# Performance work log

Hardware: AMD Instinct MI355X
Metric: run time of the kernel (lower is better)

Reference implementation:

```python
import jax, jax.numpy as jnp
import numpy as np

LOG2E = 1.4426950408889634  # 1/ln(2): convert natural-log gates to log2 space (kernel uses exp2)
BT = 64  # chunk size


def setup_inputs() -> dict:
    key = jax.random.key(0)
    ks = jax.random.split(key, 5)
    B, H, T, K, V = 4, 8, 4096, 128, 128
    return {
        "q": jax.random.normal(ks[0], (B, H, T, K), dtype=jnp.float32),
        "k": jax.random.normal(ks[1], (B, H, T, K), dtype=jnp.float32),
        "v": jax.random.normal(ks[2], (B, H, T, V), dtype=jnp.float32),
        "i_gate": jax.random.normal(ks[3], (B, H, T), dtype=jnp.float32),
        "f_gate": jax.random.normal(ks[4], (B, H, T), dtype=jnp.float32),
    }


def reference(q, k, v, i_gate, f_gate):
    B, H, T, K = q.shape
    V = v.shape[-1]
    NT = T // BT
    scale = K ** -0.5

    # gate preprocessing: log-sigmoid forget gate, both gates moved to log2 space
    vecF = jax.nn.log_sigmoid(f_gate) * LOG2E  # [B,H,T]
    vecI = i_gate * LOG2E                      # [B,H,T]

    f_c = vecF.reshape(B, H, NT, BT)
    i_c = vecI.reshape(B, H, NT, BT)
    qc = q.reshape(B, H, NT, BT, K)
    kc = k.reshape(B, H, NT, BT, K)
    vc = v.reshape(B, H, NT, BT, V)

    vecB = jnp.cumsum(f_c, axis=-1)            # inclusive cumsum of f within chunk [B,H,NT,BT]
    scaG = vecB[..., -1]                       # total decay per chunk [B,H,NT]
    vecA = i_c + (scaG[..., None] - vecB)      # i_j + sum of f after j within chunk

    # ---- inter-chunk recurrence over matrix state C, normalizer n, max m ----
    kx = jnp.moveaxis(kc, 2, 0)  # [NT,B,H,BT,K]
    vx = jnp.moveaxis(vc, 2, 0)
    ax = jnp.moveaxis(vecA, 2, 0)  # [NT,B,H,BT]
    gx = jnp.moveaxis(scaG, 2, 0)  # [NT,B,H]

    C0 = jnp.zeros((B, H, K, V), dtype=q.dtype)
    n0 = jnp.zeros((B, H, K), dtype=q.dtype)
    m0 = jnp.zeros((B, H), dtype=q.dtype)

    def step(carry, inp):
        C, n, m = carry
        kk, vv, a, g = inp
        m_next = jnp.maximum(g + m, jnp.max(a, axis=-1))      # running stabilizer max
        dec = jnp.exp2(g + m - m_next)                        # [B,H]
        kbar = kk * jnp.exp2(a - m_next[..., None])[..., None]
        C_next = C * dec[..., None, None] + jnp.einsum('bhtk,bhtv->bhkv', kbar, vv)
        n_next = n * dec[..., None] + kbar.sum(axis=-2)
        return (C_next, n_next, m_next), (C, n, m)

    _, (Cp, np_, mp) = jax.lax.scan(step, (C0, n0, m0), (kx, vx, ax, gx))
    Cp = jnp.moveaxis(Cp, 0, 2)   # state entering each chunk [B,H,NT,K,V]
    np_ = jnp.moveaxis(np_, 0, 2)  # [B,H,NT,K]
    mp = jnp.moveaxis(mp, 0, 2)   # [B,H,NT]

    # ---- intra-chunk parallel part ----
    idx = jnp.arange(BT)
    causal = idx[:, None] >= idx[None, :]  # query i attends key j<=i
    # logD[i,j] = B_i - B_j + I_j for j<=i
    logD = vecB[..., :, None] - vecB[..., None, :] + i_c[..., None, :]
    logD = jnp.where(causal, logD, -jnp.inf)
    m_intra = logD.max(axis=-1)                                   # [B,H,NT,BT]
    m_comb = jnp.maximum(mp[..., None] + vecB, m_intra)           # total stabilizer per row
    D = jnp.exp2(logD - m_comb[..., None])                        # masked entries -> 0

    S = jnp.einsum('bhcik,bhcjk->bhcij', qc, kc) * scale * D
    qbar = qc * (scale * jnp.exp2(vecB + mp[..., None] - m_comb))[..., None]

    Hnum = jnp.einsum('bhcik,bhckv->bhciv', qbar, Cp) + jnp.einsum('bhcij,bhcjv->bhciv', S, vc)
    den = jnp.einsum('bhcik,bhck->bhci', qbar, np_) + S.sum(axis=-1)
    norm = jnp.maximum(jnp.abs(den), jnp.exp2(-m_comb))
    h = Hnum / norm[..., None]
    return h.reshape(B, H, T, V)
```

## Files before the change

### kernel.cpp

```cpp
#include <hip/hip_runtime.h>
#include <hip/hip_bf16.h>
#include <math.h>


#define LOG2E 1.4426950408889634f
constexpr int Bsz = 4, Hsz = 8, Tsz = 4096, Ksz = 128, Vsz = 128;
constexpr int BT = 64, NT = 64, BH = Bsz * Hsz;
constexpr float SCALE = 0.08838834764831845f;
constexpr int CPB = 4;

typedef __attribute__((ext_vector_type(8))) short short8v;
typedef __attribute__((ext_vector_type(4))) float f32x4;
typedef __attribute__((ext_vector_type(4))) unsigned short u16x4;
typedef __attribute__((ext_vector_type(8))) unsigned short u16x8;

__device__ inline float bf2f(unsigned short u) {
    union { unsigned int i; float f; } c; c.i = ((unsigned int)u) << 16; return c.f;
}
__device__ inline unsigned short f2bf(float f) {
    __hip_bfloat16 h = __float2bfloat16(f);
    union { __hip_bfloat16 b; unsigned short u; } cv; cv.b = h; return cv.u;
}
__device__ inline float f4c(const float4& v, int y) {
    return y == 0 ? v.x : y == 1 ? v.y : y == 2 ? v.z : v.w;
}

__global__ __launch_bounds__(64) void k_gates(
    const float* __restrict__ ig, const float* __restrict__ fg,
    float* __restrict__ vecB, float* __restrict__ vecI, float* __restrict__ vecA,
    float* __restrict__ mintra, float* __restrict__ scaG, float* __restrict__ scaA)
{
    int c = blockIdx.x, bh = blockIdx.y, lane = threadIdx.x;
    int t = bh * Tsz + c * BT + lane;
    float f = fg[t];
    float ls = fminf(f, 0.f) - log1pf(expf(-fabsf(f)));
    float vF = ls * LOG2E;
    float vI = ig[t] * LOG2E;
    float b = vF;
    #pragma unroll
    for (int off = 1; off < 64; off <<= 1) {
        float o = __shfl_up(b, off, 64);
        if (lane >= off) b += o;
    }
    float g = __shfl(b, 63, 64);
    float mi = vI - b;
    #pragma unroll
    for (int off = 1; off < 64; off <<= 1) {
        float o = __shfl_up(mi, off, 64);
        if (lane >= off) mi = fmaxf(mi, o);
    }
    float a = vI + g - b;
    vecB[t] = b; vecI[t] = vI; vecA[t] = a; mintra[t] = b + mi;
    float am = a;
    #pragma unroll
    for (int off = 32; off; off >>= 1) am = fmaxf(am, __shfl_xor(am, off, 64));
    if (lane == 0) { scaG[bh * NT + c] = g; scaA[bh * NT + c] = am; }
}

__global__ __launch_bounds__(64) void k_mscan(
    const float* __restrict__ scaG, const float* __restrict__ scaA,
    float* __restrict__ mp, float* __restrict__ dec)
{
    int bh = blockIdx.x, lane = threadIdx.x;
    float g0 = scaG[bh * NT + lane];
    float a = g0, b = scaA[bh * NT + lane];
    #pragma unroll
    for (int off = 1; off < 64; off <<= 1) {
        float ap = __shfl_up(a, off, 64);
        float bp = __shfl_up(b, off, 64);
        if (lane >= off) { b = fmaxf(bp + a, b); a = ap + a; }
    }
    float m_incl = fmaxf(a, b);
    float m_prev = __shfl_up(m_incl, 1, 64);
    if (lane == 0) { m_prev = 0.f; mp[bh * (NT + 1)] = 0.f; }
    mp[bh * (NT + 1) + lane + 1] = m_incl;
    dec[bh * NT + lane] = exp2f(g0 + m_prev - m_incl);
}

__global__ __launch_bounds__(256, 2) void k_state(
    const float* __restrict__ kg, const float* __restrict__ vg,
    const float* __restrict__ vecA, const float* __restrict__ mp,
    unsigned short* __restrict__ UT, float* __restrict__ nU)
{
    int c0 = blockIdx.x * CPB, bh = blockIdx.y, tid = threadIdx.x;
    int lane = tid & 63, wid = tid >> 6;
    int lrow = lane & 15, kgrp = lane >> 4;

    __shared__ __align__(16) unsigned short kT[2][128][72];
    __shared__ __align__(16) unsigned short vT[2][128][72];
    __shared__ float nUp[2][128][5];

    int cb = tid & 15, jr = tid >> 4;
    int wboff = (((jr >> 1) ^ (cb & 7)) * 16) + (jr & 1) * 8;
    const float* mpb = mp + bh * (NT + 1);

    float4 kreg[4][2], vreg[4][2];

    auto issue_loads = [&](int cc) {
        size_t hbc = (size_t)bh * Tsz + (size_t)(c0 + cc) * BT;
        #pragma unroll
        for (int x = 0; x < 4; ++x)
            #pragma unroll
            for (int p = 0; p < 2; ++p) {
                kreg[x][p] = *(const float4*)(kg + (hbc + jr * 4 + x) * Ksz + p * 64 + cb * 4);
                vreg[x][p] = *(const float4*)(vg + (hbc + jr * 4 + x) * Vsz + p * 64 + cb * 4);
            }
    };
    auto cvt_store = [&](int cc, int b) {
        size_t hbc = (size_t)bh * Tsz + (size_t)(c0 + cc) * BT;
        float mpn = mpb[c0 + cc + 1];
        float s4[4];
        #pragma unroll
        for (int x = 0; x < 4; ++x) s4[x] = exp2f(vecA[hbc + jr * 4 + x] - mpn);
        #pragma unroll
        for (int p = 0; p < 2; ++p) {
            int cb0 = p * 64 + cb * 4;
            #pragma unroll
            for (int y = 0; y < 4; ++y) {
                u16x4 h, w;
                float psum = 0.f;
                #pragma unroll
                for (int x = 0; x < 4; ++x) {
                    float kf = f4c(kreg[x][p], y) * s4[x];
                    h[x] = f2bf(kf);
                    psum += kf;
                    w[x] = f2bf(f4c(vreg[x][p], y));
                }
                *(u16x4*)((char*)&kT[b][cb0 + y][0] + wboff) = h;
                *(u16x4*)((char*)&vT[b][cb0 + y][0] + wboff) = w;
                psum += __shfl_xor(psum, 16, 64);
                psum += __shfl_xor(psum, 32, 64);
                if (kgrp == 0) nUp[b][cb0 + y][wid] = psum;
            }
        }
    };

    issue_loads(0);
    cvt_store(0, 0);
    __syncthreads();

    int b = 0;
    for (int cc = 0; cc < CPB; ++cc) {
        if (cc + 1 < CPB) issue_loads(cc + 1);

        f32x4 acc[2][8];
        #pragma unroll
        for (int kt = 0; kt < 2; ++kt)
            #pragma unroll
            for (int vt = 0; vt < 8; ++vt) acc[kt][vt] = (f32x4){0.f, 0.f, 0.f, 0.f};
        #pragma unroll
        for (int ks = 0; ks < 2; ++ks) {
            int G = ks * 4 + kgrp;
            #pragma unroll
            for (int kt = 0; kt < 2; ++kt) {
                int arow = (wid * 2 + kt) * 16 + lrow;
                short8v af = *(const short8v*)((const char*)&kT[b][arow][0]
                                               + ((G ^ ((arow >> 2) & 7)) * 16));
                #pragma unroll
                for (int vt = 0; vt < 8; ++vt) {
                    int brow = vt * 16 + lrow;
                    short8v bv = *(const short8v*)((const char*)&vT[b][brow][0]
                                                   + ((G ^ ((brow >> 2) & 7)) * 16));
                    acc[kt][vt] = __builtin_amdgcn_mfma_f32_16x16x32_bf16(af, bv, acc[kt][vt], 0, 0, 0);
                }
            }
        }
        unsigned short* Ub = UT + (size_t)(bh * NT + c0 + cc) * (Ksz * Vsz);
        #pragma unroll
        for (int kt = 0; kt < 2; ++kt) {
            int ktile = wid * 2 + kt;
            #pragma unroll
            for (int vt = 0; vt < 8; ++vt) {
                u16x4 w;
                #pragma unroll
                for (int r = 0; r < 4; ++r) w[r] = f2bf(acc[kt][vt][r]);
                *(u16x4*)(Ub + ((size_t)(ktile * 8 + vt) * 64 + lane) * 4) = w;
            }
        }
        if (tid < Ksz) {
            float s = nUp[b][tid][0] + nUp[b][tid][1] + nUp[b][tid][2] + nUp[b][tid][3];
            nU[(size_t)(bh * NT + c0 + cc) * Ksz + tid] = s;
        }

        if (cc + 1 < CPB) {
            cvt_store(cc + 1, b ^ 1);
            __syncthreads();
            b ^= 1;
        }
    }
}

__global__ __launch_bounds__(128) void k_scan(
    unsigned short* __restrict__ UT, const float* __restrict__ dec,
    const float* __restrict__ nU, float* __restrict__ np)
{
    int s = blockIdx.x, bh = blockIdx.y, tid = threadIdx.x;
    __shared__ float decs[NT];
    if (tid < NT) decs[tid] = dec[bh * NT + tid];
    __syncthreads();
    if (s == 32) {
        float n = 0.f;
        size_t base = (size_t)bh * NT * Ksz + tid;
        #pragma unroll 4
        for (int c2 = 0; c2 < NT; ++c2) {
            float u = nU[base + (size_t)c2 * Ksz];
            np[base + (size_t)c2 * Ksz] = n;
            n = n * decs[c2] + u;
        }
        return;
    }
    size_t base = (size_t)bh * NT * (Ksz * Vsz) + s * 512 + tid * 4;
    float C0 = 0.f, C1 = 0.f, C2 = 0.f, C3 = 0.f;
    #pragma unroll 4
    for (int c2 = 0; c2 < NT; ++c2) {
        size_t idx = base + (size_t)c2 * (Ksz * Vsz);
        u16x4 u = *(const u16x4*)(UT + idx);
        u16x4 w;
        w.x = f2bf(C0); w.y = f2bf(C1); w.z = f2bf(C2); w.w = f2bf(C3);
        *(u16x4*)(UT + idx) = w;
        float d = decs[c2];
        C0 = C0 * d + bf2f(u.x); C1 = C1 * d + bf2f(u.y);
        C2 = C2 * d + bf2f(u.z); C3 = C3 * d + bf2f(u.w);
    }
}

__global__ __launch_bounds__(256, 4) void k_intra(
    const float* __restrict__ qg, const float* __restrict__ kgl, const float* __restrict__ vg,
    const float* __restrict__ vecB, const float* __restrict__ vecI,
    const float* __restrict__ mintra, const float* __restrict__ mp,
    const float* __restrict__ np, const unsigned short* __restrict__ CpT,
    float* __restrict__ out)
{
    int c = blockIdx.x, bh = blockIdx.y, tid = threadIdx.x;
    int lane = tid & 63, wid = tid >> 6;
    int lrow = lane & 15, kgrp = lane >> 4;

    __shared__ __align__(16) unsigned short R[17408];
    __shared__ float rowf[BT], colf[BT], sfqs[BT], emcs[BT], denb[BT], npv[Ksz];

    auto khi = (unsigned short(*)[136])R;
    auto klo = (unsigned short(*)[136])(R + 64 * 136);
    auto Sb  = (unsigned short(*)[72])R;
    unsigned short* vTf = R + 64 * 72;
    unsigned short* cpsF = R;

    size_t hb = (size_t)bh * Tsz + (size_t)c * BT;
    float mpc = mp[bh * (NT + 1) + c];
    if (tid < BT) {
        float b = vecB[hb + tid];
        float mc = fmaxf(mpc + b, mintra[hb + tid]);
        rowf[tid] = SCALE * exp2f(b - mc);
        colf[tid] = exp2f(vecI[hb + tid] - b);
        sfqs[tid] = SCALE * exp2f(b + mpc - mc);
        emcs[tid] = exp2f(-mc);
    }
    if (tid < Ksz) npv[tid] = np[((size_t)bh * NT + c) * Ksz + tid];

    const float4* k4 = (const float4*)(kgl + hb * Ksz);
    for (int e = tid; e < BT * Ksz / 4; e += 256) {
        int i = e >> 5, c4 = (e & 31) * 4;
        float4 kv = k4[e];
        u16x4 h, l;
        h.x = f2bf(kv.x); l.x = f2bf(kv.x - bf2f(h.x));
        h.y = f2bf(kv.y); l.y = f2bf(kv.y - bf2f(h.y));
        h.z = f2bf(kv.z); l.z = f2bf(kv.z - bf2f(h.z));
        h.w = f2bf(kv.w); l.w = f2bf(kv.w - bf2f(h.w));
        *(u16x4*)&khi[i][c4] = h; *(u16x4*)&klo[i][c4] = l;
    }
    const float* qrow = qg + (hb + wid * 16 + lrow) * Ksz;
    float qf[4][8];
    #pragma unroll
    for (int ks = 0; ks < 4; ++ks) {
        float4 a = *(const float4*)(qrow + ks * 32 + kgrp * 8);
        float4 b = *(const float4*)(qrow + ks * 32 + kgrp * 8 + 4);
        qf[ks][0] = a.x; qf[ks][1] = a.y; qf[ks][2] = a.z; qf[ks][3] = a.w;
        qf[ks][4] = b.x; qf[ks][5] = b.y; qf[ks][6] = b.z; qf[ks][7] = b.w;
    }
    int vcb = tid & 15, jb = tid >> 4;
    float vpre[2][4][4];
    #pragma unroll
    for (int p = 0; p < 2; ++p)
        #pragma unroll
        for (int x = 0; x < 4; ++x) {
            float4 r4 = *(const float4*)(vg + (hb + jb * 4 + x) * Vsz + p * 64 + vcb * 4);
            vpre[p][x][0] = r4.x; vpre[p][x][1] = r4.y; vpre[p][x][2] = r4.z; vpre[p][x][3] = r4.w;
        }
    __syncthreads();

    float dot = 0.f;
    #pragma unroll
    for (int ks = 0; ks < 4; ++ks)
        #pragma unroll
        for (int x = 0; x < 8; ++x) dot += qf[ks][x] * npv[ks * 32 + kgrp * 8 + x];
    dot += __shfl_xor(dot, 16, 64);
    dot += __shfl_xor(dot, 32, 64);
    float qdot = sfqs[wid * 16 + lrow] * dot;

    short8v qh[4], ql[4];
    #pragma unroll
    for (int ks = 0; ks < 4; ++ks)
        #pragma unroll
        for (int x = 0; x < 8; ++x) {
            float f = qf[ks][x];
            unsigned short hh = f2bf(f);
            qh[ks][x] = (short)hh;
            ql[ks][x] = (short)f2bf(f - bf2f(hh));
        }

    f32x4 accS[4];
    #pragma unroll
    for (int jt = 0; jt < 4; ++jt) accS[jt] = (f32x4){0.f, 0.f, 0.f, 0.f};
    #pragma unroll
    for (int ks = 0; ks < 4; ++ks) {
        #pragma unroll
        for (int jt = 0; jt < 4; ++jt) {
            if (jt <= wid) {
                short8v bh_ = *(const short8v*)&khi[jt * 16 + lrow][ks * 32 + kgrp * 8];
                short8v bl  = *(const short8v*)&klo[jt * 16 + lrow][ks * 32 + kgrp * 8];
                accS[jt] = __builtin_amdgcn_mfma_f32_16x16x32_bf16(qh[ks], bh_, accS[jt], 0, 0, 0);
                accS[jt] = __builtin_amdgcn_mfma_f32_16x16x32_bf16(ql[ks], bh_, accS[jt], 0, 0, 0);
                accS[jt] = __builtin_amdgcn_mfma_f32_16x16x32_bf16(qh[ks], bl,  accS[jt], 0, 0, 0);
            }
        }
    }

    float rsum[4] = {0.f, 0.f, 0.f, 0.f};
    unsigned short sreg[4][4];
    #pragma unroll
    for (int jt = 0; jt < 4; ++jt)
        #pragma unroll
        for (int r = 0; r < 4; ++r) {
            int i = wid * 16 + kgrp * 4 + r, j = jt * 16 + lrow;
            float val = (j <= i) ? accS[jt][r] * rowf[i] * colf[j] : 0.f;
            rsum[r] += val;
            sreg[jt][r] = f2bf(val);
        }
    #pragma unroll
    for (int r = 0; r < 4; ++r) {
        rsum[r] += __shfl_xor(rsum[r], 1, 64);
        rsum[r] += __shfl_xor(rsum[r], 2, 64);
        rsum[r] += __shfl_xor(rsum[r], 4, 64);
        rsum[r] += __shfl_xor(rsum[r], 8, 64);
    }
    float qd[4];
    #pragma unroll
    for (int r = 0; r < 4; ++r) qd[r] = __shfl(qdot, kgrp * 4 + r, 64);
    if (lrow == 0) {
        #pragma unroll
        for (int r = 0; r < 4; ++r) {
            int i = wid * 16 + kgrp * 4 + r;
            float den = qd[r] + rsum[r];
            denb[i] = 1.f / fmaxf(fabsf(den), emcs[i]);
        }
    }
    __syncthreads();

    const u16x8* Cg = (const u16x8*)(CpT + ((size_t)bh * NT + c) * (Ksz * Vsz));
    u16x8 cpre[8];
    #pragma unroll
    for (int p2 = 0; p2 < 8; ++p2) cpre[p2] = Cg[tid + p2 * 256];

    #pragma unroll
    for (int jt = 0; jt < 4; ++jt)
        #pragma unroll
        for (int r = 0; r < 4; ++r)
            Sb[wid * 16 + kgrp * 4 + r][jt * 16 + lrow] = sreg[jt][r];
    #pragma unroll
    for (int p = 0; p < 2; ++p)
        #pragma unroll
        for (int y = 0; y < 4; ++y) {
            int row = p * 64 + vcb * 4 + y;
            int swzb = (jb * 8) ^ ((row & 7) << 4);
            u16x4 w;
            #pragma unroll
            for (int x = 0; x < 4; ++x) w[x] = f2bf(vpre[p][x][y]);
            *(u16x4*)((char*)(vTf + row * 64) + swzb) = w;
        }
    __syncthreads();

    f32x4 accV[8];
    #pragma unroll
    for (int vt = 0; vt < 8; ++vt) accV[vt] = (f32x4){0.f, 0.f, 0.f, 0.f};
    #pragma unroll
    for (int ks = 0; ks < 2; ++ks) {
        short8v as_ = *(const short8v*)&Sb[wid * 16 + lrow][ks * 32 + kgrp * 8];
        #pragma unroll
        for (int vt = 0; vt < 8; ++vt) {
            int row = vt * 16 + lrow;
            int swzb = ((ks * 64 + kgrp * 16)) ^ ((row & 7) << 4);
            short8v bv = *(const short8v*)((const char*)(vTf + row * 64) + swzb);
            accV[vt] = __builtin_amdgcn_mfma_f32_16x16x32_bf16(as_, bv, accV[vt], 0, 0, 0);
        }
    }
    __syncthreads();

    #pragma unroll
    for (int p2 = 0; p2 < 8; ++p2) {
        int idx = tid + p2 * 256;
        *(u16x8*)&cpsF[idx * 8] = cpre[p2];
    }
    __syncthreads();

    f32x4 accC[8];
    #pragma unroll
    for (int vt = 0; vt < 8; ++vt) accC[vt] = (f32x4){0.f, 0.f, 0.f, 0.f};
    #pragma unroll
    for (int ks = 0; ks < 4; ++ks) {
        int ktile = ks * 2 + (kgrp >> 1);
        int lsrc = (kgrp & 1) * 32 + lrow;
        #pragma unroll
        for (int vt = 0; vt < 8; ++vt) {
            const unsigned short* pf = &cpsF[((ktile * 8 + vt) * 64 + lsrc) * 4];
            u16x4 lo4 = *(const u16x4*)pf;
            u16x4 hi4 = *(const u16x4*)(pf + 64);
            short8v bc;
            bc[0] = (short)lo4.x; bc[1] = (short)lo4.y; bc[2] = (short)lo4.z; bc[3] = (short)lo4.w;
            bc[4] = (short)hi4.x; bc[5] = (short)hi4.y; bc[6] = (short)hi4.z; bc[7] = (short)hi4.w;
            accC[vt] = __builtin_amdgcn_mfma_f32_16x16x32_bf16(qh[ks], bc, accC[vt], 0, 0, 0);
            accC[vt] = __builtin_amdgcn_mfma_f32_16x16x32_bf16(ql[ks], bc, accC[vt], 0, 0, 0);
        }
    }
    size_t gb = hb * Vsz;
    #pragma unroll
    for (int vt = 0; vt < 8; ++vt)
        #pragma unroll
        for (int r = 0; r < 4; ++r) {
            int i = wid * 16 + kgrp * 4 + r, vc = vt * 16 + lrow;
            out[gb + (size_t)i * Vsz + vc] = (sfqs[i] * accC[vt][r] + accV[vt][r]) * denb[i];
        }
}

extern "C" void kernel_launch(void* const* d_in, const int* in_sizes, int n_in,
                              void* d_out, int out_size, void* d_ws, size_t ws_size,
                              hipStream_t stream) {
    const float* q  = (const float*)d_in[0];
    const float* k  = (const float*)d_in[1];
    const float* v  = (const float*)d_in[2];
    const float* ig = (const float*)d_in[3];
    const float* fg = (const float*)d_in[4];
    float* out = (float*)d_out;

    float* ws = (float*)d_ws;
    float* vecB   = ws;
    float* vecI   = vecB + BH * Tsz;
    float* vecA   = vecI + BH * Tsz;
    float* mintra = vecA + BH * Tsz;
    float* scaG   = mintra + BH * Tsz;
    float* scaA   = scaG + BH * NT;
    float* dec    = scaA + BH * NT;
    float* mp     = dec + BH * NT;
    float* nU     = mp + BH * (NT + 1);
    float* np     = nU + BH * NT * Ksz;
    unsigned short* UT = (unsigned short*)(np + BH * NT * Ksz);

    k_gates<<<dim3(NT, BH), 64, 0, stream>>>(ig, fg, vecB, vecI, vecA, mintra, scaG, scaA);
    k_mscan<<<dim3(BH), 64, 0, stream>>>(scaG, scaA, mp, dec);
    k_state<<<dim3(NT / CPB, BH), 256, 0, stream>>>(k, v, vecA, mp, UT, nU);
    k_scan<<<dim3(33, BH), 128, 0, stream>>>(UT, dec, nU, np);
    k_intra<<<dim3(NT, BH), 256, 0, stream>>>(q, k, v, vecB, vecI, mintra, mp, np, UT, out);
}
```

Baseline: 124.9 us.

## Replace flat chunk-state scan with two-level grouped scan and in-block local recurrence

Each k_state block now runs the state recurrence across a group of 8 chunks in registers, emitting per-chunk local states and a group-total state. A short scan over 8 group states replaces the 64-step global scan, which removes the serial scan and its round-trip through the per-chunk update buffer. k_intra combines the local state with the decayed group prefix using precomputed decay factors. This costs a second state load and an extra 128x128 MFMA pass per chunk in k_intra, and k_state launches fewer blocks (8 per head instead of 16) with longer serial work, so there is less parallelism.

```diff
diff --git a/kernel.cpp b/kernel.cpp
--- a/kernel.cpp
+++ b/kernel.cpp
@@ -7,7 +7,7 @@
 constexpr int Bsz = 4, Hsz = 8, Tsz = 4096, Ksz = 128, Vsz = 128;
 constexpr int BT = 64, NT = 64, BH = Bsz * Hsz;
 constexpr float SCALE = 0.08838834764831845f;
-constexpr int CPB = 4;
+constexpr int GS = 8, NG = NT / GS;
 
 typedef __attribute__((ext_vector_type(8))) short short8v;
 typedef __attribute__((ext_vector_type(4))) float f32x4;
@@ -59,7 +59,8 @@
 
 __global__ __launch_bounds__(64) void k_mscan(
     const float* __restrict__ scaG, const float* __restrict__ scaA,
-    float* __restrict__ mp, float* __restrict__ dec)
+    float* __restrict__ mp, float* __restrict__ dec,
+    float* __restrict__ pdec, float* __restrict__ decG)
 {
     int bh = blockIdx.x, lane = threadIdx.x;
     float g0 = scaG[bh * NT + lane];
@@ -75,14 +76,28 @@
     if (lane == 0) { m_prev = 0.f; mp[bh * (NT + 1)] = 0.f; }
     mp[bh * (NT + 1) + lane + 1] = m_incl;
     dec[bh * NT + lane] = exp2f(g0 + m_prev - m_incl);
-}
-
-__global__ __launch_bounds__(256, 2) void k_state(
+    float cumE = a - g0;
+    int gs = lane & ~(GS - 1);
+    float cumE_gs = __shfl(cumE, gs, 64);
+    float mp_gs   = __shfl(m_prev, gs, 64);
+    pdec[bh * NT + lane] = exp2f(cumE - cumE_gs + mp_gs - m_prev);
+    int ge = (lane * GS) & 63, gl = (lane * GS + GS - 1) & 63;
+    float cumS = __shfl(cumE, ge, 64);
+    float mS   = __shfl(m_prev, ge, 64);
+    float cumL = __shfl(a, gl, 64);
+    float mL   = __shfl(m_incl, gl, 64);
+    if (lane < NG) decG[bh * NG + lane] = exp2f(cumL - cumS + mS - mL);
+}
+
+__global__ __launch_bounds__(256, 1) void k_state(
     const float* __restrict__ kg, const float* __restrict__ vg,
     const float* __restrict__ vecA, const float* __restrict__ mp,
-    unsigned short* __restrict__ UT, float* __restrict__ nU)
+    const float* __restrict__ dec,
+    unsigned short* __restrict__ CpL, unsigned short* __restrict__ Gb,
+    float* __restrict__ npl, float* __restrict__ nG)
 {
-    int c0 = blockIdx.x * CPB, bh = blockIdx.y, tid = threadIdx.x;
+    int g = blockIdx.x, bh = blockIdx.y, tid = threadIdx.x;
+    int c0 = g * GS;
     int lane = tid & 63, wid = tid >> 6;
     int lrow = lane & 15, kgrp = lane >> 4;
 
@@ -95,7 +110,6 @@
     const float* mpb = mp + bh * (NT + 1);
 
     float4 kreg[4][2], vreg[4][2];
-
     auto issue_loads = [&](int cc) {
         size_t hbc = (size_t)bh * Tsz + (size_t)(c0 + cc) * BT;
         #pragma unroll
@@ -106,7 +120,7 @@
                 vreg[x][p] = *(const float4*)(vg + (hbc + jr * 4 + x) * Vsz + p * 64 + cb * 4);
             }
     };
-    auto cvt_store = [&](int cc, int b) {
+    auto cvt_store = [&](int cc, int bb) {
         size_t hbc = (size_t)bh * Tsz + (size_t)(c0 + cc) * BT;
         float mpn = mpb[c0 + cc + 1];
         float s4[4];
@@ -114,7 +128,7 @@
         for (int x = 0; x < 4; ++x) s4[x] = exp2f(vecA[hbc + jr * 4 + x] - mpn);
         #pragma unroll
         for (int p = 0; p < 2; ++p) {
-            int cb0 = p * 64 + cb * 4;
+            int cc0 = p * 64 + cb * 4;
             #pragma unroll
             for (int y = 0; y < 4; ++y) {
                 u16x4 h, w;
@@ -126,11 +140,11 @@
                     psum += kf;
                     w[x] = f2bf(f4c(vreg[x][p], y));
                 }
-                *(u16x4*)((char*)&kT[b][cb0 + y][0] + wboff) = h;
-                *(u16x4*)((char*)&vT[b][cb0 + y][0] + wboff) = w;
+                *(u16x4*)((char*)&kT[bb][cc0 + y][0] + wboff) = h;
+                *(u16x4*)((char*)&vT[bb][cc0 + y][0] + wboff) = w;
                 psum += __shfl_xor(psum, 16, 64);
                 psum += __shfl_xor(psum, 32, 64);
-                if (kgrp == 0) nUp[b][cb0 + y][wid] = psum;
+                if (kgrp == 0) nUp[bb][cc0 + y][wid] = psum;
             }
         }
     };
@@ -139,33 +153,18 @@
     cvt_store(0, 0);
     __syncthreads();
 
-    int b = 0;
-    for (int cc = 0; cc < CPB; ++cc) {
-        if (cc + 1 < CPB) issue_loads(cc + 1);
-
-        f32x4 acc[2][8];
-        #pragma unroll
-        for (int kt = 0; kt < 2; ++kt)
-            #pragma unroll
-            for (int vt = 0; vt < 8; ++vt) acc[kt][vt] = (f32x4){0.f, 0.f, 0.f, 0.f};
-        #pragma unroll
-        for (int ks = 0; ks < 2; ++ks) {
-            int G = ks * 4 + kgrp;
-            #pragma unroll
-            for (int kt = 0; kt < 2; ++kt) {
-                int arow = (wid * 2 + kt) * 16 + lrow;
-                short8v af = *(const short8v*)((const char*)&kT[b][arow][0]
-                                               + ((G ^ ((arow >> 2) & 7)) * 16));
-                #pragma unroll
-                for (int vt = 0; vt < 8; ++vt) {
-                    int brow = vt * 16 + lrow;
-                    short8v bv = *(const short8v*)((const char*)&vT[b][brow][0]
-                                                   + ((G ^ ((brow >> 2) & 7)) * 16));
-                    acc[kt][vt] = __builtin_amdgcn_mfma_f32_16x16x32_bf16(af, bv, acc[kt][vt], 0, 0, 0);
-                }
-            }
-        }
-        unsigned short* Ub = UT + (size_t)(bh * NT + c0 + cc) * (Ksz * Vsz);
+    f32x4 acc[2][8];
+    #pragma unroll
+    for (int kt = 0; kt < 2; ++kt)
+        #pragma unroll
+        for (int vt = 0; vt < 8; ++vt) acc[kt][vt] = (f32x4){0.f, 0.f, 0.f, 0.f};
+    float n_own = 0.f;
+
+    int bb = 0;
+    for (int t = 0; t < GS; ++t) {
+        if (t + 1 < GS) issue_loads(t + 1);
+        int c = c0 + t;
+        unsigned short* Cb = CpL + (size_t)(bh * NT + c) * (Ksz * Vsz);
         #pragma unroll
         for (int kt = 0; kt < 2; ++kt) {
             int ktile = wid * 2 + kt;
@@ -174,51 +173,88 @@
                 u16x4 w;
                 #pragma unroll
                 for (int r = 0; r < 4; ++r) w[r] = f2bf(acc[kt][vt][r]);
-                *(u16x4*)(Ub + ((size_t)(ktile * 8 + vt) * 64 + lane) * 4) = w;
+                *(u16x4*)(Cb + ((size_t)(ktile * 8 + vt) * 64 + lane) * 4) = w;
             }
         }
+        if (tid < Ksz) npl[(size_t)(bh * NT + c) * Ksz + tid] = n_own;
+        float dct = dec[bh * NT + c];
+        #pragma unroll
+        for (int kt = 0; kt < 2; ++kt)
+            #pragma unroll
+            for (int vt = 0; vt < 8; ++vt)
+                #pragma unroll
+                for (int r = 0; r < 4; ++r) acc[kt][vt][r] *= dct;
+        #pragma unroll
+        for (int ks = 0; ks < 2; ++ks) {
+            int G2 = ks * 4 + kgrp;
+            #pragma unroll
+            for (int kt = 0; kt < 2; ++kt) {
+                int arow = (wid * 2 + kt) * 16 + lrow;
+                short8v af = *(const short8v*)((const char*)&kT[bb][arow][0]
+                                               + ((G2 ^ ((arow >> 2) & 7)) * 16));
+                #pragma unroll
+                for (int vt = 0; vt < 8; ++vt) {
+                    int brow = vt * 16 + lrow;
+                    short8v bv = *(const short8v*)((const char*)&vT[bb][brow][0]
+                                                   + ((G2 ^ ((brow >> 2) & 7)) * 16));
+                    acc[kt][vt] = __builtin_amdgcn_mfma_f32_16x16x32_bf16(af, bv, acc[kt][vt], 0, 0, 0);
+                }
+            }
+        }
         if (tid < Ksz) {
-            float s = nUp[b][tid][0] + nUp[b][tid][1] + nUp[b][tid][2] + nUp[b][tid][3];
-            nU[(size_t)(bh * NT + c0 + cc) * Ksz + tid] = s;
-        }
-
-        if (cc + 1 < CPB) {
-            cvt_store(cc + 1, b ^ 1);
+            float s = nUp[bb][tid][0] + nUp[bb][tid][1] + nUp[bb][tid][2] + nUp[bb][tid][3];
+            n_own = n_own * dct + s;
+        }
+        if (t + 1 < GS) {
+            cvt_store(t + 1, bb ^ 1);
             __syncthreads();
-            b ^= 1;
-        }
-    }
-}
-
-__global__ __launch_bounds__(128) void k_scan(
-    unsigned short* __restrict__ UT, const float* __restrict__ dec,
-    const float* __restrict__ nU, float* __restrict__ np)
+            bb ^= 1;
+        }
+    }
+    unsigned short* Gg = Gb + (size_t)(bh * NG + g) * (Ksz * Vsz);
+    #pragma unroll
+    for (int kt = 0; kt < 2; ++kt) {
+        int ktile = wid * 2 + kt;
+        #pragma unroll
+        for (int vt = 0; vt < 8; ++vt) {
+            u16x4 w;
+            #pragma unroll
+            for (int r = 0; r < 4; ++r) w[r] = f2bf(acc[kt][vt][r]);
+            *(u16x4*)(Gg + ((size_t)(ktile * 8 + vt) * 64 + lane) * 4) = w;
+        }
+    }
+    if (tid < Ksz) nG[(size_t)(bh * NG + g) * Ksz + tid] = n_own;
+}
+
+__global__ __launch_bounds__(128) void k_gscan(
+    unsigned short* __restrict__ Gb, float* __restrict__ nG,
+    const float* __restrict__ decG)
 {
     int s = blockIdx.x, bh = blockIdx.y, tid = threadIdx.x;
-    __shared__ float decs[NT];
-    if (tid < NT) decs[tid] = dec[bh * NT + tid];
+    __shared__ float dgs[NG];
+    if (tid < NG) dgs[tid] = decG[bh * NG + tid];
     __syncthreads();
     if (s == 32) {
         float n = 0.f;
-        size_t base = (size_t)bh * NT * Ksz + tid;
-        #pragma unroll 4
-        for (int c2 = 0; c2 < NT; ++c2) {
-            float u = nU[base + (size_t)c2 * Ksz];
-            np[base + (size_t)c2 * Ksz] = n;
-            n = n * decs[c2] + u;
+        size_t base = (size_t)bh * NG * Ksz + tid;
+        #pragma unroll
+        for (int g = 0; g < NG; ++g) {
+            float u = nG[base + (size_t)g * Ksz];
+            nG[base + (size_t)g * Ksz] = n;
+            n = n * dgs[g] + u;
         }
         return;
     }
-    size_t base = (size_t)bh * NT * (Ksz * Vsz) + s * 512 + tid * 4;
+    size_t base = (size_t)bh * NG * (Ksz * Vsz) + s * 512 + tid * 4;
     float C0 = 0.f, C1 = 0.f, C2 = 0.f, C3 = 0.f;
-    #pragma unroll 4
-    for (int c2 = 0; c2 < NT; ++c2) {
-        size_t idx = base + (size_t)c2 * (Ksz * Vsz);
-        u16x4 u = *(const u16x4*)(UT + idx);
+    #pragma unroll
+    for (int g = 0; g < NG; ++g) {
+        size_t idx = base + (size_t)g * (Ksz * Vsz);
+        u16x4 u = *(const u16x4*)(Gb + idx);
         u16x4 w;
         w.x = f2bf(C0); w.y = f2bf(C1); w.z = f2bf(C2); w.w = f2bf(C3);
-        *(u16x4*)(UT + idx) = w;
-        float d = decs[c2];
+        *(u16x4*)(Gb + idx) = w;
+        float d = dgs[g];
         C0 = C0 * d + bf2f(u.x); C1 = C1 * d + bf2f(u.y);
         C2 = C2 * d + bf2f(u.z); C3 = C3 * d + bf2f(u.w);
     }
@@ -228,12 +264,14 @@
     const float* __restrict__ qg, const float* __restrict__ kgl, const float* __restrict__ vg,
     const float* __restrict__ vecB, const float* __restrict__ vecI,
     const float* __restrict__ mintra, const float* __restrict__ mp,
-    const float* __restrict__ np, const unsigned short* __restrict__ CpT,
-    float* __restrict__ out)
+    const float* __restrict__ npl, const float* __restrict__ nB,
+    const unsigned short* __restrict__ CpL, const unsigned short* __restrict__ Bb,
+    const float* __restrict__ pdec, float* __restrict__ out)
 {
     int c = blockIdx.x, bh = blockIdx.y, tid = threadIdx.x;
     int lane = tid & 63, wid = tid >> 6;
     int lrow = lane & 15, kgrp = lane >> 4;
+    int grp = c / GS;
 
     __shared__ __align__(16) unsigned short R[17408];
     __shared__ float rowf[BT], colf[BT], sfqs[BT], emcs[BT], denb[BT], npv[Ksz];
@@ -246,6 +284,7 @@
 
     size_t hb = (size_t)bh * Tsz + (size_t)c * BT;
     float mpc = mp[bh * (NT + 1) + c];
+    float pd = pdec[bh * NT + c];
     if (tid < BT) {
         float b = vecB[hb + tid];
         float mc = fmaxf(mpc + b, mintra[hb + tid]);
@@ -254,7 +293,9 @@
         sfqs[tid] = SCALE * exp2f(b + mpc - mc);
         emcs[tid] = exp2f(-mc);
     }
-    if (tid < Ksz) npv[tid] = np[((size_t)bh * NT + c) * Ksz + tid];
+    if (tid < Ksz)
+        npv[tid] = npl[((size_t)bh * NT + c) * Ksz + tid]
+                 + pd * nB[((size_t)bh * NG + grp) * Ksz + tid];
 
     const float4* k4 = (const float4*)(kgl + hb * Ksz);
     for (int e = tid; e < BT * Ksz / 4; e += 256) {
@@ -355,10 +396,11 @@
     }
     __syncthreads();
 
-    const u16x8* Cg = (const u16x8*)(CpT + ((size_t)bh * NT + c) * (Ksz * Vsz));
-    u16x8 cpre[8];
-    #pragma unroll
-    for (int p2 = 0; p2 < 8; ++p2) cpre[p2] = Cg[tid + p2 * 256];
+    const u16x8* Cg = (const u16x8*)(CpL + ((size_t)bh * NT + c) * (Ksz * Vsz));
+    const u16x8* Bg = (const u16x8*)(Bb + ((size_t)bh * NG + grp) * (Ksz * Vsz));
+    u16x8 cpre[8], bpre[8];
+    #pragma unroll
+    for (int p2 = 0; p2 < 8; ++p2) { cpre[p2] = Cg[tid + p2 * 256]; bpre[p2] = Bg[tid + p2 * 256]; }
 
     #pragma unroll
     for (int jt = 0; jt < 4; ++jt)
@@ -400,7 +442,6 @@
         *(u16x8*)&cpsF[idx * 8] = cpre[p2];
     }
     __syncthreads();
-
     f32x4 accC[8];
     #pragma unroll
     for (int vt = 0; vt < 8; ++vt) accC[vt] = (f32x4){0.f, 0.f, 0.f, 0.f};
@@ -420,13 +461,42 @@
             accC[vt] = __builtin_amdgcn_mfma_f32_16x16x32_bf16(ql[ks], bc, accC[vt], 0, 0, 0);
         }
     }
+    __syncthreads();
+
+    #pragma unroll
+    for (int p2 = 0; p2 < 8; ++p2) {
+        int idx = tid + p2 * 256;
+        *(u16x8*)&cpsF[idx * 8] = bpre[p2];
+    }
+    __syncthreads();
+    f32x4 accB[8];
+    #pragma unroll
+    for (int vt = 0; vt < 8; ++vt) accB[vt] = (f32x4){0.f, 0.f, 0.f, 0.f};
+    #pragma unroll
+    for (int ks = 0; ks < 4; ++ks) {
+        int ktile = ks * 2 + (kgrp >> 1);
+        int lsrc = (kgrp & 1) * 32 + lrow;
+        #pragma unroll
+        for (int vt = 0; vt < 8; ++vt) {
+            const unsigned short* pf = &cpsF[((ktile * 8 + vt) * 64 + lsrc) * 4];
+            u16x4 lo4 = *(const u16x4*)pf;
+            u16x4 hi4 = *(const u16x4*)(pf + 64);
+            short8v bc;
+            bc[0] = (short)lo4.x; bc[1] = (short)lo4.y; bc[2] = (short)lo4.z; bc[3] = (short)lo4.w;
+            bc[4] = (short)hi4.x; bc[5] = (short)hi4.y; bc[6] = (short)hi4.z; bc[7] = (short)hi4.w;
+            accB[vt] = __builtin_amdgcn_mfma_f32_16x16x32_bf16(qh[ks], bc, accB[vt], 0, 0, 0);
+            accB[vt] = __builtin_amdgcn_mfma_f32_16x16x32_bf16(ql[ks], bc, accB[vt], 0, 0, 0);
+        }
+    }
+
     size_t gb = hb * Vsz;
     #pragma unroll
     for (int vt = 0; vt < 8; ++vt)
         #pragma unroll
         for (int r = 0; r < 4; ++r) {
             int i = wid * 16 + kgrp * 4 + r, vc = vt * 16 + lrow;
-            out[gb + (size_t)i * Vsz + vc] = (sfqs[i] * accC[vt][r] + accV[vt][r]) * denb[i];
+            float inter = accC[vt][r] + pd * accB[vt][r];
+            out[gb + (size_t)i * Vsz + vc] = (sfqs[i] * inter + accV[vt][r]) * denb[i];
         }
 }
 
@@ -448,14 +518,18 @@
     float* scaG   = mintra + BH * Tsz;
     float* scaA   = scaG + BH * NT;
     float* dec    = scaA + BH * NT;
-    float* mp     = dec + BH * NT;
-    float* nU     = mp + BH * (NT + 1);
-    float* np     = nU + BH * NT * Ksz;
-    unsigned short* UT = (unsigned short*)(np + BH * NT * Ksz);
+    float* pdec   = dec + BH * NT;
+    float* decG   = pdec + BH * NT;
+    float* mp     = decG + BH * NG;
+    float* npl    = mp + BH * (NT + 1);
+    float* nG     = npl + BH * NT * Ksz;
+    unsigned short* CpL = (unsigned short*)(nG + BH * NG * Ksz);
+    unsigned short* Gb  = CpL + (size_t)BH * NT * Ksz * Vsz;
 
     k_gates<<<dim3(NT, BH), 64, 0, stream>>>(ig, fg, vecB, vecI, vecA, mintra, scaG, scaA);
-    k_mscan<<<dim3(BH), 64, 0, stream>>>(scaG, scaA, mp, dec);
-    k_state<<<dim3(NT / CPB, BH), 256, 0, stream>>>(k, v, vecA, mp, UT, nU);
-    k_scan<<<dim3(33, BH), 128, 0, stream>>>(UT, dec, nU, np);
-    k_intra<<<dim3(NT, BH), 256, 0, stream>>>(q, k, v, vecB, vecI, mintra, mp, np, UT, out);
-}
+    k_mscan<<<dim3(BH), 64, 0, stream>>>(scaG, scaA, mp, dec, pdec, decG);
+    k_state<<<dim3(NG, BH), 256, 0, stream>>>(k, v, vecA, mp, dec, CpL, Gb, npl, nG);
+    k_gscan<<<dim3(33, BH), 128, 0, stream>>>(Gb, nG, decG);
+    k_intra<<<dim3(NT, BH), 256, 0, stream>>>(q, k, v, vecB, vecI, mintra, mp,
+                                              npl, nG, CpL, Gb, pdec, out);
+}
```

Result: slower. 174.4 us (+39.6%).
